# Performance work log

Hardware: AMD Instinct MI355X
Metric: run time of the kernel (lower is better)

## Reference

```python
import math
import jax, jax.numpy as jnp
import numpy as np

B, L, D, H = 2, 2048, 1024, 16
DK = D // H
N_TYPES = 6  # token types; < 3 => prompt (U/O/E), >= 3 => item (I)


def setup_inputs() -> dict:
    key = jax.random.key(0)
    ks = jax.random.split(key, 8)
    w_scale = 0.02
    return {
        "x": jax.random.normal(ks[0], (B, L, D), dtype=jnp.float32),
        "token_types": jax.random.randint(ks[1], (B, L), 0, N_TYPES, dtype=jnp.int32),
        "seq_lens": jax.random.randint(ks[2], (B,), L // 2, L + 1, dtype=jnp.int32),
        "W_q": jax.random.normal(ks[3], (D, D), dtype=jnp.float32) * w_scale,
        "W_k": jax.random.normal(ks[4], (D, D), dtype=jnp.float32) * w_scale,
        "W_v": jax.random.normal(ks[5], (D, D), dtype=jnp.float32) * w_scale,
        "W_u": jax.random.normal(ks[6], (D, D), dtype=jnp.float32) * w_scale,
        "W_o": jax.random.normal(ks[7], (D, D), dtype=jnp.float32) * w_scale,
    }


def reference(x, token_types, seq_lens, W_q, W_k, W_v, W_u, W_o):
    b, l, d = x.shape
    neg = jnp.finfo(x.dtype).min

    def proj(W):  # torch Linear (no bias): y = x @ W.T -> (b, H, l, dk)
        return jnp.einsum("bld,ed->ble", x, W).reshape(b, l, H, DK).transpose(0, 2, 1, 3)

    Q, K, V, U = proj(W_q), proj(W_k), proj(W_v), proj(W_u)

    scores = jnp.einsum("bhid,bhjd->bhij", Q, K) / math.sqrt(DK)  # (b,H,l,l)

    # Hybrid mask: causal (-inf above diagonal), but 0 wherever key j is a
    # prompt token (prompt<->prompt bidirectional, item->prompt allowed).
    is_prompt = token_types < 3                      # (b, l)
    causal = jnp.where(jnp.triu(jnp.ones((l, l), dtype=bool), k=1), neg, 0.0).astype(x.dtype)
    mask = jnp.where(is_prompt[:, None, :], jnp.asarray(0.0, x.dtype), causal[None, :, :])  # (b,l,l)
    scores = scores + mask[:, None, :, :]

    # Padding mask on key positions j >= seq_len
    pad = jnp.arange(l)[None, :] >= seq_lens[:, None]  # (b, l)
    scores = jnp.where(pad[:, None, None, :], neg, scores)

    attn = jax.nn.softmax(scores, axis=-1)
    out = jnp.einsum("bhij,bhjd->bhid", attn, V) * U   # HSTU pointwise gating
    out = out.transpose(0, 2, 1, 3).reshape(b, l, d)
    return jnp.einsum("bld,ed->ble", out, W_o)
```

## Files before the change

kernel.cpp:

```cpp
#include <hip/hip_runtime.h>


#define L_SEQ 2048

typedef __attribute__((ext_vector_type(8))) short bf16x8;
typedef __attribute__((ext_vector_type(8))) unsigned short u16x8;
typedef __attribute__((ext_vector_type(4))) float f32x4;
typedef __attribute__((ext_vector_type(16))) float f32x16;

#if __has_builtin(__builtin_amdgcn_exp2f)
#define EXP2F __builtin_amdgcn_exp2f
#else
#define EXP2F __builtin_exp2f
#endif

__device__ __forceinline__ unsigned short f2bf(float f) {
  union { float f; unsigned u; } c; c.f = f;
  unsigned r = c.u + 0x7FFFu + ((c.u >> 16) & 1u);
  return (unsigned short)(r >> 16);
}
__device__ __forceinline__ float bf2f(unsigned short h) {
  union { unsigned u; float f; } c; c.u = ((unsigned)h) << 16;
  return c.f;
}

__device__ __forceinline__ void async16(const void* g, void* l) {
  __builtin_amdgcn_global_load_lds((__attribute__((address_space(1))) void*)g,
                                   (__attribute__((address_space(3))) void*)l,
                                   16, 0, 0);
}

__device__ __forceinline__ unsigned cvtpk_bf16(float lo, float hi) {
  unsigned r; asm("v_cvt_pk_bf16_f32 %0, %1, %2" : "=v"(r) : "v"(lo), "v"(hi));
  return r;
}

__global__ __launch_bounds__(256) void cvt_all(
    const float* __restrict__ x,
    const float* __restrict__ wq, const float* __restrict__ wk,
    const float* __restrict__ wv, const float* __restrict__ wu,
    const float* __restrict__ wo,
    unsigned short* __restrict__ xb, unsigned short* __restrict__ wcat) {
  const int seg = blockIdx.x >> 10;
  const float* s;
  unsigned short* d;
  float sc = 1.0f;
  if (seg < 4)      { s = x + (size_t)seg * 1048576;  d = xb + (size_t)seg * 1048576; }
  else {
    const int ws = seg - 4;
    s = ws == 0 ? wq : ws == 1 ? wk : ws == 2 ? wv : ws == 3 ? wu : wo;
    d = wcat + (size_t)ws * 1048576;
    if (ws == 0) sc = 0.18033688011112042f;
  }
  const int i = ((blockIdx.x & 1023) * 256 + threadIdx.x) * 4;
  const float4 v = *reinterpret_cast<const float4*>(s + i);
  ushort4 o;
  o.x = f2bf(v.x * sc); o.y = f2bf(v.y * sc); o.z = f2bf(v.z * sc); o.w = f2bf(v.w * sc);
  *reinterpret_cast<ushort4*>(d + i) = o;
}

__global__ __launch_bounds__(256) void vtrans(const unsigned short* __restrict__ qkvu,
                                              unsigned short* __restrict__ vtg,
                                              const int* __restrict__ tt,
                                              const int* __restrict__ sl,
                                              unsigned* __restrict__ allowed) {
  __shared__ unsigned short tileb[4096];
  const int t = blockIdx.x, h = blockIdx.y, b = blockIdx.z;
  const size_t rb = (size_t)b * L_SEQ * 4096;
  const int tid = threadIdx.x;
  const int vp = tid & 31, vd0 = (tid >> 5) * 8;
  const int j0 = t * 64;
  if (h == 0 && tid < 64) {
    const int j = j0 + tid;
    const unsigned long long m = __ballot((tt[b * L_SEQ + j] < 3) && (j < sl[b]));
    if (tid == 0) {
      allowed[b * 64 + 2 * t]     = (unsigned)m;
      allowed[b * 64 + 2 * t + 1] = (unsigned)(m >> 32);
    }
  }
  const u16x8 g0 = *reinterpret_cast<const u16x8*>(
      qkvu + rb + (size_t)(j0 + 2 * vp) * 4096 + 2048 + h * 64 + vd0);
  const u16x8 g1 = *reinterpret_cast<const u16x8*>(
      qkvu + rb + (size_t)(j0 + 2 * vp + 1) * 4096 + 2048 + h * 64 + vd0);
  #pragma unroll
  for (int e = 0; e < 8; ++e) {
    const int d = vd0 + e;
    const unsigned pk = (unsigned)g0[e] | ((unsigned)g1[e] << 16);
    *reinterpret_cast<unsigned*>((char*)tileb +
        d * 128 + 16 * ((vp >> 2) ^ (d & 7)) + 4 * (vp & 3)) = pk;
  }
  __syncthreads();
  const size_t ob = ((size_t)(b * 16 + h) * 32 + t) * 4096;
  *reinterpret_cast<u16x8*>(vtg + ob + tid * 16) =
      *reinterpret_cast<const u16x8*>(tileb + tid * 16);
  *reinterpret_cast<u16x8*>(vtg + ob + tid * 16 + 8) =
      *reinterpret_cast<const u16x8*>(tileb + tid * 16 + 8);
}

template<int OUT_BF16>
__global__ __launch_bounds__(256) void gemm_bt(
    const unsigned short* __restrict__ A,
    const unsigned short* __restrict__ BT,
    float* __restrict__ Cf, unsigned short* __restrict__ Cb,
    int M, int N, int K, int cpx, int nbxm, int nbxs)
{
  __shared__ unsigned short As[2][128 * 32];
  __shared__ unsigned short Bs[2][128 * 32];

  const int tid = threadIdx.x;
  const int w = tid >> 6, lane = tid & 63;
  const int lo = lane & 15, hi = lane >> 4;
  const int d = blockIdx.x + gridDim.x * blockIdx.y;
  const int lin = (d & 7) * cpx + (d >> 3);
  const int i0 = (lin >> nbxs) * 128, j0 = (lin & nbxm) * 128;
  const int wr = w >> 1, wc = w & 1;
  const int c0 = w * 2, rsub = lane >> 2, csub = (lane & 3) * 8;

  f32x4 acc[4][4] = {};

  #pragma unroll
  for (int q = 0; q < 2; ++q) {
    const int c = c0 + q;
    async16(A  + (size_t)(i0 + c * 16 + rsub) * K + csub, &As[0][c * 512]);
    async16(BT + (size_t)(j0 + c * 16 + rsub) * K + csub, &Bs[0][c * 512]);
  }
  __syncthreads();

  const int nt = K >> 5;
  for (int t = 0; t < nt; ++t) {
    const int buf = t & 1;
    if (t + 1 < nt) {
      const int k0 = (t + 1) << 5;
      #pragma unroll
      for (int q = 0; q < 2; ++q) {
        const int c = c0 + q;
        async16(A  + (size_t)(i0 + c * 16 + rsub) * K + k0 + csub, &As[buf ^ 1][c * 512]);
        async16(BT + (size_t)(j0 + c * 16 + rsub) * K + k0 + csub, &Bs[buf ^ 1][c * 512]);
      }
    }
    bf16x8 a[4], b[4];
    #pragma unroll
    for (int m = 0; m < 4; ++m)
      a[m] = *reinterpret_cast<const bf16x8*>(&As[buf][(wr * 64 + m * 16 + lo) * 32 + hi * 8]);
    #pragma unroll
    for (int n = 0; n < 4; ++n)
      b[n] = *reinterpret_cast<const bf16x8*>(&Bs[buf][(wc * 64 + n * 16 + lo) * 32 + hi * 8]);
    #pragma unroll
    for (int m = 0; m < 4; ++m)
      #pragma unroll
      for (int n = 0; n < 4; ++n)
        acc[m][n] = __builtin_amdgcn_mfma_f32_16x16x32_bf16(a[m], b[n], acc[m][n], 0, 0, 0);
    __syncthreads();
  }

  #pragma unroll
  for (int m = 0; m < 4; ++m) {
    const int row = i0 + wr * 64 + m * 16 + hi * 4;
    #pragma unroll
    for (int n = 0; n < 4; ++n) {
      const int col = j0 + wc * 64 + n * 16 + lo;
      #pragma unroll
      for (int r = 0; r < 4; ++r) {
        if (OUT_BF16) Cb[(size_t)(row + r) * N + col] = f2bf(acc[m][n][r]);
        else          Cf[(size_t)(row + r) * N + col] = acc[m][n][r];
      }
    }
  }
}

__global__ __launch_bounds__(512, 4) void hstu_attn(
    const unsigned short* __restrict__ qkvu,
    const unsigned short* __restrict__ vtg,
    const unsigned* __restrict__ allowed,
    const int* __restrict__ slens,
    unsigned short* __restrict__ gated)
{
  __shared__ char smem[65536];

  const int dlin = blockIdx.x + (blockIdx.y << 4) + (blockIdx.z << 8);
  const int lin = ((dlin & 7) << 6) | (dlin >> 3);
  const int qt = lin & 15, h = (lin >> 4) & 15, b = lin >> 8;
  const int i0 = qt * 128;
  const int tid = threadIdx.x, w = tid >> 6, lane = tid & 63;
  const int g = w >> 2, wq = w & 3;
  const int c = lane & 31, sb = lane >> 5;
  const int seqlen = slens[b];
  const size_t rb = (size_t)b * L_SEQ * 4096;
  const size_t vb = (size_t)(b * 16 + h) * 32 * 4096;
  const int qrow = i0 + wq * 32 + c;

  auto stageK = [&](int buf, int t) {
    const int j0 = t * 64;
    char* Kb = smem + (g * 2 + buf) * 8192;
    #pragma unroll
    for (int q = 0; q < 2; ++q) {
      const int p = wq * 2 + q;
      const int krow = 8 * p + (lane >> 3);
      const int d0 = 8 * ((lane & 7) ^ (lane >> 3));
      async16(qkvu + rb + (size_t)(j0 + krow) * 4096 + 1024 + h * 64 + d0,
              Kb + p * 1024);
    }
  };
  auto stageV = [&](int buf, int t) {
    char* Vb = smem + 32768 + (g * 2 + buf) * 8192;
    #pragma unroll
    for (int q = 0; q < 2; ++q) {
      const int p = wq * 2 + q;
      async16(vtg + vb + (size_t)t * 4096 + p * 512 + lane * 8, Vb + p * 1024);
    }
  };

  const int nt = (seqlen + 63) >> 6;
  const int niter = (nt + 1) >> 1;

  stageK(0, g); stageV(0, g);

  bf16x8 qf[4];
  #pragma unroll
  for (int kd = 0; kd < 4; ++kd)
    qf[kd] = *reinterpret_cast<const bf16x8*>(
        qkvu + rb + (size_t)qrow * 4096 + h * 64 + kd * 16 + sb * 8);
  const unsigned pmword = allowed[b * 64 + lane];
  const int limb = (qrow < seqlen - 1 ? qrow : seqlen - 1) - 4 * sb;

  f32x16 o0 = {}, o1 = {};
  float rs = 0.f;

  asm volatile("s_waitcnt vmcnt(0)" ::: "memory");
  __builtin_amdgcn_s_barrier();
  __builtin_amdgcn_sched_barrier(0);

  for (int i = 0; i < niter; ++i) {
    const int t = 2 * i + g;
    const bool active = t < nt;
    const int buf = i & 1;
    const int j0 = t * 64;
    const bool pre = (t + 2 < nt);

    if (active) {
      if (pre) { stageK(buf ^ 1, t + 2); stageV(buf ^ 1, t + 2); }

      const char* Kb = smem + (g * 2 + buf) * 8192;
      const char* Vb = smem + 32768 + (g * 2 + buf) * 8192;
      const bool fast = (j0 + 64 <= seqlen) && (j0 + 63 <= i0 + wq * 32);

      #pragma unroll
      for (int z = 0; z < 2; ++z) {
        f32x16 s = {};
        __builtin_amdgcn_s_setprio(1);
        #pragma unroll
        for (int kd = 0; kd < 4; ++kd) {
          const bf16x8 kf = *reinterpret_cast<const bf16x8*>(
              Kb + (32 * z + c) * 128 + (((2 * kd + sb) ^ (c & 7)) << 4));
          s = __builtin_amdgcn_mfma_f32_32x32x16_bf16(kf, qf[kd], s, 0, 0, 0);
        }
        __builtin_amdgcn_s_setprio(0);

        if (fast) {
          #pragma unroll
          for (int r = 0; r < 16; ++r) { s[r] = EXP2F(s[r]); rs += s[r]; }
        } else {
          const unsigned pmz = __builtin_amdgcn_readlane(pmword, 2 * t + z);
          const int lim = limb - j0 - 32 * z;
          const unsigned cm = lim < 0 ? 0u : (lim >= 31 ? ~0u : ((2u << lim) - 1u));
          const unsigned al = (pmz >> (4 * sb)) | cm;
          #pragma unroll
          for (int r = 0; r < 16; ++r) {
            const int kc = (r & 3) + 8 * (r >> 2);
            const float p = EXP2F(s[r]);
            s[r] = ((al >> kc) & 1) ? p : 0.f;
            rs += s[r];
          }
        }

        unsigned U0, U1, W0, W1;
        U0 = cvtpk_bf16(s[0], s[1]);  U1 = cvtpk_bf16(s[2], s[3]);
        W0 = cvtpk_bf16(s[4], s[5]);  W1 = cvtpk_bf16(s[6], s[7]);
        asm("v_permlane32_swap_b32 %0, %1" : "+v"(U0), "+v"(W0));
        asm("v_permlane32_swap_b32 %0, %1" : "+v"(U1), "+v"(W1));
        union { unsigned u[4]; bf16x8 v; } pu;
        pu.u[0] = U0; pu.u[1] = U1; pu.u[2] = W0; pu.u[3] = W1;
        const bf16x8 pfE = pu.v;
        U0 = cvtpk_bf16(s[8], s[9]);   U1 = cvtpk_bf16(s[10], s[11]);
        W0 = cvtpk_bf16(s[12], s[13]); W1 = cvtpk_bf16(s[14], s[15]);
        asm("v_permlane32_swap_b32 %0, %1" : "+v"(U0), "+v"(W0));
        asm("v_permlane32_swap_b32 %0, %1" : "+v"(U1), "+v"(W1));
        pu.u[0] = U0; pu.u[1] = U1; pu.u[2] = W0; pu.u[3] = W1;
        const bf16x8 pfO = pu.v;

        const int kpE = 2 * z, kpO = 2 * z + 1;
        const int swE = ((2 * kpE + sb) ^ (c & 7)) << 4;
        const int swO = ((2 * kpO + sb) ^ (c & 7)) << 4;
        const bf16x8 ve0 = *reinterpret_cast<const bf16x8*>(Vb + c * 128 + swE);
        const bf16x8 ve1 = *reinterpret_cast<const bf16x8*>(Vb + (32 + c) * 128 + swE);
        const bf16x8 vo0 = *reinterpret_cast<const bf16x8*>(Vb + c * 128 + swO);
        const bf16x8 vo1 = *reinterpret_cast<const bf16x8*>(Vb + (32 + c) * 128 + swO);
        __builtin_amdgcn_s_setprio(1);
        o0 = __builtin_amdgcn_mfma_f32_32x32x16_bf16(ve0, pfE, o0, 0, 0, 0);
        o1 = __builtin_amdgcn_mfma_f32_32x32x16_bf16(ve1, pfE, o1, 0, 0, 0);
        o0 = __builtin_amdgcn_mfma_f32_32x32x16_bf16(vo0, pfO, o0, 0, 0, 0);
        o1 = __builtin_amdgcn_mfma_f32_32x32x16_bf16(vo1, pfO, o1, 0, 0, 0);
        __builtin_amdgcn_s_setprio(0);
      }
      asm volatile("s_waitcnt vmcnt(0)" ::: "memory");
    }
    __builtin_amdgcn_s_barrier();
    __builtin_amdgcn_sched_barrier(0);
  }

  const float lsum = rs + __shfl_xor(rs, 32, 64);

  float* cb = (float*)smem;
  const int col = wq * 64 + lane;
  if (g == 1) {
    #pragma unroll
    for (int r = 0; r < 16; ++r) {
      cb[r * 260 + col]        = o0[r];
      cb[(16 + r) * 260 + col] = o1[r];
    }
    cb[32 * 260 + col] = lsum;
  }
  __syncthreads();
  if (g == 1) return;
  #pragma unroll
  for (int r = 0; r < 16; ++r) {
    o0[r] += cb[r * 260 + col];
    o1[r] += cb[(16 + r) * 260 + col];
  }
  const float rin = 1.0f / (lsum + cb[32 * 260 + col]);

  #pragma unroll
  for (int n = 0; n < 2; ++n) {
    const f32x16 o = n ? o1 : o0;
    #pragma unroll
    for (int rq = 0; rq < 4; ++rq) {
      const int d0 = n * 32 + 8 * rq + 4 * sb;
      const ushort4 uu = *reinterpret_cast<const ushort4*>(
          qkvu + rb + (size_t)qrow * 4096 + 3072 + h * 64 + d0);
      ushort4 gg;
      gg.x = f2bf(o[4 * rq + 0] * rin * bf2f(uu.x));
      gg.y = f2bf(o[4 * rq + 1] * rin * bf2f(uu.y));
      gg.z = f2bf(o[4 * rq + 2] * rin * bf2f(uu.z));
      gg.w = f2bf(o[4 * rq + 3] * rin * bf2f(uu.w));
      *reinterpret_cast<ushort4*>(
          gated + (size_t)(b * L_SEQ + qrow) * 1024 + h * 64 + d0) = gg;
    }
  }
}

extern "C" void kernel_launch(void* const* d_in, const int* in_sizes, int n_in,
                              void* d_out, int out_size, void* d_ws, size_t ws_size,
                              hipStream_t stream) {
  const float* x  = (const float*)d_in[0];
  const int* tt   = (const int*)d_in[1];
  const int* sl   = (const int*)d_in[2];
  const float* Wq = (const float*)d_in[3];
  const float* Wk = (const float*)d_in[4];
  const float* Wv = (const float*)d_in[5];
  const float* Wu = (const float*)d_in[6];
  const float* Wo = (const float*)d_in[7];
  float* out = (float*)d_out;

  unsigned* allowed     = (unsigned*)d_ws;
  unsigned short* xb    = (unsigned short*)d_ws + 256;
  unsigned short* wcat  = xb    + (size_t)4096 * 1024;
  unsigned short* wob   = wcat  + (size_t)4096 * 1024;
  unsigned short* qkvu  = wob   + (size_t)1024 * 1024;
  unsigned short* gated = qkvu  + (size_t)4096 * 4096;
  unsigned short* vtg   = xb;

  cvt_all<<<9216, 256, 0, stream>>>(x, Wq, Wk, Wv, Wu, Wo, xb, wcat);

  gemm_bt<1><<<dim3(32, 32), 256, 0, stream>>>(xb, wcat, nullptr, qkvu,
                                               4096, 4096, 1024, 128, 31, 5);

  vtrans<<<dim3(32, 16, 2), 256, 0, stream>>>(qkvu, vtg, tt, sl, allowed);

  hstu_attn<<<dim3(16, 16, 2), 512, 0, stream>>>(qkvu, vtg, allowed, sl, gated);

  gemm_bt<0><<<dim3(8, 32), 256, 0, stream>>>(gated, wob, out, nullptr,
                                              4096, 1024, 1024, 32, 7, 3);
}
```

Baseline: 141.3 us.

## Use 256x256-tile async-copy GEMM for fused QKVU projection

Replaces the 128x128-tile QKVU projection GEMM with a new 256x256-tile kernel using 512 threads, async global-to-LDS copies with double buffering, XOR-swizzled LDS layout, and MFMA 16x16x32 bf16 with setprio phases. The larger tile raises arithmetic intensity and cuts redundant global loads, and the async staging overlaps loads with compute. In exchange it uses 128KB of shared memory and only 256 blocks, which may limit occupancy or leave some CUs underused. Its output stores are scalar 2-byte writes, which may be uncoalesced.

```diff
diff --git a/kernel.cpp b/kernel.cpp
--- a/kernel.cpp
+++ b/kernel.cpp
@@ -97,6 +97,105 @@
       *reinterpret_cast<const u16x8*>(tileb + tid * 16 + 8);
 }
 
+__global__ __launch_bounds__(512, 2) void gemm256_bt(
+    const unsigned short* __restrict__ A,
+    const unsigned short* __restrict__ BT,
+    unsigned short* __restrict__ Cb, int K, int N)
+{
+  __shared__ char smem[131072];
+
+  const int tid = threadIdx.x, w = tid >> 6, lane = tid & 63;
+  const int lo = lane & 15, hi = lane >> 4;
+  const int wm = w >> 2, wn = w & 3;
+  const int d = blockIdx.x;
+  const int lin = (d & 7) * 32 + (d >> 3);
+  const int i0 = (lin >> 4) * 256, j0 = (lin & 15) * 256;
+
+  const int rr = lane >> 3, ch = lane & 7;
+  const int ksw = 8 * (ch ^ rr);
+
+  auto stage = [&](int buf, int t) {
+    const size_t k0 = (size_t)t * 64 + ksw;
+    #pragma unroll
+    for (int q = 0; q < 2; ++q) {
+      const int p = 2 * w + q;
+      const int row = 8 * p + rr;
+      #pragma unroll
+      for (int h = 0; h < 2; ++h) {
+        async16(A  + (size_t)(i0 + h * 128 + row) * K + k0,
+                smem + buf * 32768 + h * 16384 + p * 1024);
+        async16(BT + (size_t)(j0 + h * 128 + row) * K + k0,
+                smem + 65536 + buf * 32768 + h * 16384 + p * 1024);
+      }
+    }
+  };
+
+  f32x4 acc[8][4] = {};
+  stage(0, 0);
+
+  const int nt = K >> 6;
+  for (int u = 0; u < nt; ++u) {
+    const int buf = u & 1;
+    if (u + 1 < nt) {
+      stage(buf ^ 1, u + 1);
+      asm volatile("s_waitcnt vmcnt(8)" ::: "memory");
+    } else {
+      asm volatile("s_waitcnt vmcnt(0)" ::: "memory");
+    }
+    __builtin_amdgcn_s_barrier();
+    __builtin_amdgcn_sched_barrier(0);
+
+    const char* Ah = smem + buf * 32768 + wm * 16384;
+    const char* Bh = smem + 65536 + buf * 32768 + (wn >> 1) * 16384;
+    const int brow0 = (wn & 1) * 64;
+
+    bf16x8 bfr[4][2];
+    #pragma unroll
+    for (int n = 0; n < 4; ++n)
+      #pragma unroll
+      for (int ks = 0; ks < 2; ++ks)
+        bfr[n][ks] = *reinterpret_cast<const bf16x8*>(
+            Bh + (brow0 + n * 16 + lo) * 128 + 16 * ((ks * 4 + hi) ^ (lo & 7)));
+
+    #pragma unroll
+    for (int ph = 0; ph < 4; ++ph) {
+      bf16x8 afr[2][2];
+      #pragma unroll
+      for (int mm = 0; mm < 2; ++mm)
+        #pragma unroll
+        for (int ks = 0; ks < 2; ++ks)
+          afr[mm][ks] = *reinterpret_cast<const bf16x8*>(
+              Ah + ((ph * 2 + mm) * 16 + lo) * 128 + 16 * ((ks * 4 + hi) ^ (lo & 7)));
+      __builtin_amdgcn_s_barrier();
+      __builtin_amdgcn_sched_barrier(0);
+      __builtin_amdgcn_s_setprio(1);
+      #pragma unroll
+      for (int ks = 0; ks < 2; ++ks)
+        #pragma unroll
+        for (int mm = 0; mm < 2; ++mm)
+          #pragma unroll
+          for (int n = 0; n < 4; ++n)
+            acc[ph * 2 + mm][n] = __builtin_amdgcn_mfma_f32_16x16x32_bf16(
+                afr[mm][ks], bfr[n][ks], acc[ph * 2 + mm][n], 0, 0, 0);
+      __builtin_amdgcn_s_setprio(0);
+      __builtin_amdgcn_s_barrier();
+      __builtin_amdgcn_sched_barrier(0);
+    }
+  }
+
+  #pragma unroll
+  for (int m = 0; m < 8; ++m) {
+    const int row = i0 + wm * 128 + m * 16 + hi * 4;
+    #pragma unroll
+    for (int n = 0; n < 4; ++n) {
+      const int col = j0 + wn * 64 + n * 16 + lo;
+      #pragma unroll
+      for (int r = 0; r < 4; ++r)
+        Cb[(size_t)(row + r) * N + col] = f2bf(acc[m][n][r]);
+    }
+  }
+}
+
 template<int OUT_BF16>
 __global__ __launch_bounds__(256) void gemm_bt(
     const unsigned short* __restrict__ A,
@@ -371,8 +470,7 @@
 
   cvt_all<<<9216, 256, 0, stream>>>(x, Wq, Wk, Wv, Wu, Wo, xb, wcat);
 
-  gemm_bt<1><<<dim3(32, 32), 256, 0, stream>>>(xb, wcat, nullptr, qkvu,
-                                               4096, 4096, 1024, 128, 31, 5);
+  gemm256_bt<<<256, 512, 0, stream>>>(xb, wcat, qkvu, 1024, 4096);
 
   vtrans<<<dim3(32, 16, 2), 256, 0, stream>>>(qkvu, vtg, tt, sl, allowed);
 
```

Measured after the change: 127.9 us. 1.1x faster.
